# Performance work log

Hardware: AMD Instinct MI355X
Metric: run time of the kernel (lower is better)

The kernel has to match this reference:

```python
import jax, jax.numpy as jnp
import numpy as np

B, T, N, H = 256, 128, 512, 128  # batch, timesteps, input_size (driving series), hidden


def setup_inputs() -> dict:
    key = jax.random.key(0)
    ks = jax.random.split(key, 7)
    p = lambda k, shape: (jax.random.normal(k, shape, dtype=jnp.float32) * 0.05)
    return {
        "X": jax.random.normal(ks[0], (B, T, N), dtype=jnp.float32),
        # attention linear: in_features = 2H + T, out_features = 1 (stored as a vector + scalar bias)
        "attn_w": p(ks[1], (2 * H + T,)),
        "attn_b": p(ks[2], ()),
        # LSTM cell params, PyTorch layout/gate order (i, f, g, o)
        "w_ih": p(ks[3], (4 * H, N)),
        "w_hh": p(ks[4], (4 * H, H)),
        "b_ih": p(ks[5], (4 * H,)),
        "b_hh": p(ks[6], (4 * H,)),
    }


def reference(X, attn_w, attn_b, w_ih, w_hh, b_ih, b_hh):
    Bn, Tn, Nn = X.shape
    Hh = w_hh.shape[1]
    # split the single attention weight row into the h / s / X-row pieces of the concat
    w_h, w_s, w_x = attn_w[:Hh], attn_w[Hh:2 * Hh], attn_w[2 * Hh:]
    Xp = jnp.swapaxes(X, 1, 2)            # [B, N, T]  (X.permute(0,2,1))
    x_score = Xp @ w_x                    # [B, N], time-invariant part of attention logits

    def step(carry, x_t):                 # x_t: [B, N] = X[:, t, :]
        h, c = carry
        # logits[b,i] = w_h.h[b] + w_s.c[b] + w_x.Xp[b,i] + b  (== Linear on the concat)
        score = x_score + (h @ w_h + c @ w_s + attn_b)[:, None]   # [B, N]
        alpha = jax.nn.softmax(score, axis=1)
        x_tilde = alpha * x_t                                      # [B, N]
        gates = x_tilde @ w_ih.T + h @ w_hh.T + b_ih + b_hh        # [B, 4H]
        i, f, g, o = jnp.split(gates, 4, axis=1)
        c_new = jax.nn.sigmoid(f) * c + jax.nn.sigmoid(i) * jnp.tanh(g)
        h_new = jax.nn.sigmoid(o) * jnp.tanh(c_new)
        return (h_new, c_new), (x_tilde, h_new)

    h0 = jnp.zeros((Bn, Hh), X.dtype)
    (_, _), (Xt, Xe) = jax.lax.scan(step, (h0, h0), jnp.swapaxes(X, 0, 1))
    # scan stacks along time -> [T, B, .]; return [B, T, .]
    return jnp.swapaxes(Xt, 0, 1), jnp.swapaxes(Xe, 0, 1)
```

## Files before the change

kernel.cpp:

```cpp
#include <hip/hip_runtime.h>
#include <hip/hip_bf16.h>

#define Bb 256
#define Tt 128
#define Nn 512
#define Hh 128

typedef __attribute__((ext_vector_type(4))) float floatx4;
typedef __attribute__((ext_vector_type(8))) short short8;
typedef _Float16 h2v_t __attribute__((ext_vector_type(2)));

__device__ __forceinline__ unsigned short f2bf(float f) {
  unsigned u = __float_as_uint(f);
  u += 0x7fffu + ((u >> 16) & 1u);
  return (unsigned short)(u >> 16);
}

__device__ __forceinline__ float sigmoid_fast(float x) {
  return __builtin_amdgcn_rcpf(1.f + __expf(-x));
}
__device__ __forceinline__ float tanh_fast(float x) {
  float e = __expf(2.f * x);
  return 1.f - 2.f * __builtin_amdgcn_rcpf(e + 1.f);
}

__device__ __forceinline__ void lds_barrier() {
  asm volatile("s_waitcnt lgkmcnt(0)" ::: "memory");
  __builtin_amdgcn_s_barrier();
  asm volatile("" ::: "memory");
}

__device__ __forceinline__ void async_load16(const void* g, void* lds) {
  __builtin_amdgcn_global_load_lds(
      (const __attribute__((address_space(1))) unsigned int*)g,
      (__attribute__((address_space(3))) unsigned int*)lds, 16, 0, 0);
}

#if __has_builtin(__builtin_amdgcn_fdot2)
#define FDOT2(a, b, c) __builtin_amdgcn_fdot2((a), (b), (c), false)
#else
__device__ __forceinline__ float fdot2_sw(h2v_t a, h2v_t b, float c) {
  return fmaf((float)a.x, (float)b.x, fmaf((float)a.y, (float)b.y, (c)));
}
#define FDOT2(a, b, c) fdot2_sw((a), (b), (c))
#endif

template <int CTRL>
__device__ __forceinline__ float qperm(float x) {
#if __has_builtin(__builtin_amdgcn_update_dpp)
  return __uint_as_float((unsigned)__builtin_amdgcn_update_dpp(
      0, (int)__float_as_uint(x), CTRL, 0xf, 0xf, true));
#else
  return __shfl_xor(x, CTRL == 0xB1 ? 1 : 2, 64);
#endif
}

__global__ void prep_kernel(const float* __restrict__ w_ih,
                            const float* __restrict__ b_ih,
                            const float* __restrict__ b_hh,
                            unsigned short* __restrict__ wb,
                            float* __restrict__ bias) {
  int i = blockIdx.x * 256 + threadIdx.x;
  if (i < 4 * Hh * Nn) wb[i] = f2bf(w_ih[i]);
  if (i < 4 * Hh) bias[i] = b_ih[i] + b_hh[i];
}

__global__ __launch_bounds__(512) void alpha_kernel(const float* __restrict__ X,
                                                    const float* __restrict__ attn_w,
                                                    float* __restrict__ alpha) {
  int b = blockIdx.x;
  int tid = threadIdx.x;
  int c = tid & 127;
  int tp = tid >> 7;
  const float4* Xb = (const float4*)(X + (size_t)b * Tt * Nn) + c;
  const float* wx = attn_w + 2 * Hh;

  float4 acc = {0.f, 0.f, 0.f, 0.f};
#pragma unroll 8
  for (int tt = 0; tt < 32; ++tt) {
    int t = tp * 32 + tt;
    float4 x = Xb[(size_t)t * 128];
    float w = wx[t];
    acc.x = fmaf(x.x, w, acc.x);
    acc.y = fmaf(x.y, w, acc.y);
    acc.z = fmaf(x.z, w, acc.z);
    acc.w = fmaf(x.w, w, acc.w);
  }

  __shared__ float4 s4[512];
  __shared__ float sred[128];
  s4[tid] = acc;
  __syncthreads();

  float4 sc = {0.f, 0.f, 0.f, 0.f};
  if (tid < 128) {
    float4 a = s4[tid], b2 = s4[tid + 128], c2 = s4[tid + 256], d = s4[tid + 384];
    sc.x = a.x + b2.x + c2.x + d.x;
    sc.y = a.y + b2.y + c2.y + d.y;
    sc.z = a.z + b2.z + c2.z + d.z;
    sc.w = a.w + b2.w + c2.w + d.w;
    sred[tid] = fmaxf(fmaxf(sc.x, sc.y), fmaxf(sc.z, sc.w));
  }
  __syncthreads();
  for (int s = 64; s > 0; s >>= 1) {
    if (tid < s) sred[tid] = fmaxf(sred[tid], sred[tid + s]);
    __syncthreads();
  }
  float m = sred[0];
  __syncthreads();

  float4 e4 = {0.f, 0.f, 0.f, 0.f};
  if (tid < 128) {
    e4.x = __expf(sc.x - m);
    e4.y = __expf(sc.y - m);
    e4.z = __expf(sc.z - m);
    e4.w = __expf(sc.w - m);
    sred[tid] = e4.x + e4.y + e4.z + e4.w;
  }
  __syncthreads();
  for (int s = 64; s > 0; s >>= 1) {
    if (tid < s) sred[tid] += sred[tid + s];
    __syncthreads();
  }
  float inv = 1.f / sred[0];
  if (tid < 128) {
    float4 out;
    out.x = e4.x * inv; out.y = e4.y * inv; out.z = e4.z * inv; out.w = e4.w * inv;
    ((float4*)(alpha + (size_t)b * Nn))[tid] = out;
  }
}

__global__ __launch_bounds__(256) void scale_kernel(const float* __restrict__ X,
                                                    const float* __restrict__ alpha,
                                                    float* __restrict__ Xt,
                                                    unsigned short* __restrict__ xtb) {
  size_t i = (size_t)blockIdx.x * 256 + threadIdx.x;
  size_t e = i * 4;
  int n = (int)(e & (Nn - 1));
  int brow = (int)(e >> 9);
  int b = brow >> 7;
  float4 x = ((const float4*)X)[i];
  float4 a = *(const float4*)(alpha + (size_t)b * Nn + n);
  float4 y;
  y.x = x.x * a.x; y.y = x.y * a.y; y.z = x.z * a.z; y.w = x.w * a.w;
  ((float4*)Xt)[i] = y;
  ushort4 u;
  u.x = f2bf(y.x); u.y = f2bf(y.y); u.z = f2bf(y.z); u.w = f2bf(y.w);
  ((ushort4*)xtb)[i] = u;
}

#define GBK 64

__global__ __launch_bounds__(256) void gemm_bt(const unsigned short* __restrict__ A,
                                               const unsigned short* __restrict__ Bw,
                                               const float* __restrict__ bias,
                                               float* __restrict__ C) {
  __shared__ __align__(16) unsigned short As[128 * 64];
  __shared__ __align__(16) unsigned short Bs[128 * 64];
  const int K = 512, NO = 512;
  int tid = threadIdx.x;
  int lane = tid & 63;
  int wave = tid >> 6;
  int wm = wave & 1, wn = wave >> 1;
  int l15 = lane & 15;
  int quad = lane >> 4;
  int mtile = blockIdx.x, ntile = blockIdx.y;

  floatx4 acc[4][4];
#pragma unroll
  for (int i = 0; i < 4; ++i)
#pragma unroll
    for (int j = 0; j < 4; ++j) acc[i][j] = (floatx4){0.f, 0.f, 0.f, 0.f};

  int lr = lane >> 3;
  int lc = (lane & 7) ^ lr;
  const size_t lane_goff = (size_t)lr * K + lc * 8;
  const size_t abase = (size_t)mtile * 128 * K + lane_goff;
  const size_t bbase = (size_t)ntile * 128 * K + lane_goff;
  int sw = (quad ^ (l15 & 7)) * 8;

  for (int kb = 0; kb < K; kb += GBK) {
#pragma unroll
    for (int slot = 0; slot < 4; ++slot) {
      int r0 = slot * 32 + wave * 8;
      async_load16(A + abase + (size_t)r0 * K + kb, &As[r0 * 64]);
      async_load16(Bw + bbase + (size_t)r0 * K + kb, &Bs[r0 * 64]);
    }
    __syncthreads();
#pragma unroll
    for (int kh = 0; kh < 2; ++kh) {
      int sc = sw ^ (kh * 32);
      short8 af[4], bf[4];
#pragma unroll
      for (int i = 0; i < 4; ++i)
        af[i] = *(const short8*)(&As[(wm * 64 + i * 16 + l15) * 64 + sc]);
#pragma unroll
      for (int j = 0; j < 4; ++j)
        bf[j] = *(const short8*)(&Bs[(wn * 64 + j * 16 + l15) * 64 + sc]);
#pragma unroll
      for (int i = 0; i < 4; ++i)
#pragma unroll
        for (int j = 0; j < 4; ++j)
          acc[i][j] = __builtin_amdgcn_mfma_f32_16x16x32_bf16(af[i], bf[j], acc[i][j], 0, 0, 0);
    }
    __syncthreads();
  }

  int m0 = mtile * 128 + wm * 64;
  int n0 = ntile * 128 + wn * 64;
#pragma unroll
  for (int j = 0; j < 4; ++j) {
    int col = n0 + j * 16 + l15;
    float bsum = bias[col];
#pragma unroll
    for (int i = 0; i < 4; ++i) {
      int row = m0 + i * 16 + quad * 4;
#pragma unroll
      for (int r = 0; r < 4; ++r)
        C[(size_t)(row + r) * NO + col] = acc[i][j][r] + bsum;
    }
  }
}

__global__ __launch_bounds__(512, 1) void lstm_kernel(const float* __restrict__ G,
                                                      const float* __restrict__ w_hh,
                                                      float* __restrict__ Xe) {
  int b = blockIdx.x;
  int tid = threadIdx.x;
  int u = tid >> 2;
  int q = tid & 3;

  h2v_t wreg[4][16];
#pragma unroll
  for (int f = 0; f < 4; ++f) {
    const float4* wr = (const float4*)(w_hh + ((size_t)(f * 128 + u) * 128 + q * 32));
#pragma unroll
    for (int i = 0; i < 8; ++i) {
      float4 v = wr[i];
      wreg[f][2 * i]     = (h2v_t){(_Float16)v.x, (_Float16)v.y};
      wreg[f][2 * i + 1] = (h2v_t){(_Float16)v.z, (_Float16)v.w};
    }
  }

  __shared__ __align__(16) unsigned short h2[2][128];
  if (tid < 128) h2[0][tid] = 0;
  __syncthreads();

  const float* Gb = G + (size_t)b * Tt * 512 + q * 128 + u;
  float* Xeb = Xe + (size_t)b * Tt * Hh;

  float gcur = Gb[0];
  float gnext = Gb[512];
  float c0 = 0.f;

#define H2F(W) __builtin_bit_cast(h2v_t, (W))

  for (int t = 0; t < Tt; ++t) {
    int cur = t & 1;
    const uint4* hp = (const uint4*)(&h2[cur][0]) + q * 4;
    uint4 ha = hp[0], hb = hp[1], hc = hp[2], hd = hp[3];

    float g_this = gcur;
    gcur = gnext;
    if (t + 2 < Tt) gnext = Gb[(size_t)(t + 2) * 512];

    float pg0 = (q == 0) ? g_this : 0.f;
    float pg1 = (q == 1) ? g_this : 0.f;
    float pg2 = (q == 2) ? g_this : 0.f;
    float pg3 = (q == 3) ? g_this : 0.f;

#define DOTK(HB, K2)                                                \
  {                                                                 \
    h2v_t hh = __builtin_bit_cast(h2v_t, (HB));                     \
    pg0 = FDOT2(hh, wreg[0][K2], pg0);                              \
    pg1 = FDOT2(hh, wreg[1][K2], pg1);                              \
    pg2 = FDOT2(hh, wreg[2][K2], pg2);                              \
    pg3 = FDOT2(hh, wreg[3][K2], pg3);                              \
  }
    DOTK(ha.x, 0)  DOTK(ha.y, 1)  DOTK(ha.z, 2)  DOTK(ha.w, 3)
    DOTK(hb.x, 4)  DOTK(hb.y, 5)  DOTK(hb.z, 6)  DOTK(hb.w, 7)
    DOTK(hc.x, 8)  DOTK(hc.y, 9)  DOTK(hc.z, 10) DOTK(hc.w, 11)
    DOTK(hd.x, 12) DOTK(hd.y, 13) DOTK(hd.z, 14) DOTK(hd.w, 15)
#undef DOTK

    pg0 += qperm<0xB1>(pg0); pg1 += qperm<0xB1>(pg1);
    pg2 += qperm<0xB1>(pg2); pg3 += qperm<0xB1>(pg3);
    pg0 += qperm<0x4E>(pg0); pg1 += qperm<0x4E>(pg1);
    pg2 += qperm<0x4E>(pg2); pg3 += qperm<0x4E>(pg3);

    float si = sigmoid_fast(pg0);
    float sf = sigmoid_fast(pg1);
    float tg = tanh_fast(pg2);
    float so = sigmoid_fast(pg3);
    c0 = sf * c0 + si * tg;
    float hv = so * tanh_fast(c0);

    if (q == 0) {
      Xeb[(size_t)t * Hh + u] = hv;
      h2[cur ^ 1][u] = __builtin_bit_cast(unsigned short, (_Float16)hv);
    }
    lds_barrier();
  }
#undef H2F
}

extern "C" void kernel_launch(void* const* d_in, const int* in_sizes, int n_in,
                              void* d_out, int out_size, void* d_ws, size_t ws_size,
                              hipStream_t stream) {
  const float* X      = (const float*)d_in[0];
  const float* attn_w = (const float*)d_in[1];
  const float* w_ih   = (const float*)d_in[3];
  const float* w_hh   = (const float*)d_in[4];
  const float* b_ih   = (const float*)d_in[5];
  const float* b_hh   = (const float*)d_in[6];

  float* Xt = (float*)d_out;
  float* Xe = (float*)d_out + (size_t)Bb * Tt * Nn;

  char* ws = (char*)d_ws;
  float*          alpha = (float*)(ws);
  float*          bias  = (float*)(ws + 524288);
  unsigned short* wb    = (unsigned short*)(ws + 526336);
  unsigned short* xtb   = (unsigned short*)(ws + 1050624);
  float*          G     = (float*)(ws + 34605056);

  prep_kernel<<<dim3(1024), dim3(256), 0, stream>>>(w_ih, b_ih, b_hh, wb, bias);
  alpha_kernel<<<dim3(Bb), dim3(512), 0, stream>>>(X, attn_w, alpha);
  scale_kernel<<<dim3(16384), dim3(256), 0, stream>>>(X, alpha, Xt, xtb);
  gemm_bt<<<dim3(256, 4), dim3(256), 0, stream>>>(xtb, wb, bias, G);
  lstm_kernel<<<dim3(Bb), dim3(512), 0, stream>>>(G, w_hh, Xe);
}
```

Before: 272.0 us.

## Fuse input-projection GEMM into LSTM kernel with producer/consumer warp specialization

Replaces the separate bf16 GEMM that writes the gate pre-activations G to global memory, and the recurrent LSTM kernel, with one 1024-thread block per batch element. Eight waves compute 16-timestep chunks of x_tilde @ w_ih^T into a double-buffered LDS tile. The other eight waves run the recurrence on the previous chunk, so the GEMM overlaps the serial LSTM steps and the G round-trip through HBM goes away. In exchange, every block reloads the full w_ih matrix from global/L2 for each chunk. It also uses about 148KB of LDS, limiting occupancy to one block per CU, and adds a block-wide barrier on every step.

```diff
diff --git a/kernel.cpp b/kernel.cpp
--- a/kernel.cpp
+++ b/kernel.cpp
@@ -22,12 +22,6 @@
 __device__ __forceinline__ float tanh_fast(float x) {
   float e = __expf(2.f * x);
   return 1.f - 2.f * __builtin_amdgcn_rcpf(e + 1.f);
-}
-
-__device__ __forceinline__ void lds_barrier() {
-  asm volatile("s_waitcnt lgkmcnt(0)" ::: "memory");
-  __builtin_amdgcn_s_barrier();
-  asm volatile("" ::: "memory");
 }
 
 __device__ __forceinline__ void async_load16(const void* g, void* lds) {
@@ -149,125 +143,135 @@
   ((ushort4*)xtb)[i] = u;
 }
 
-#define GBK 64
-
-__global__ __launch_bounds__(256) void gemm_bt(const unsigned short* __restrict__ A,
-                                               const unsigned short* __restrict__ Bw,
-                                               const float* __restrict__ bias,
-                                               float* __restrict__ C) {
-  __shared__ __align__(16) unsigned short As[128 * 64];
-  __shared__ __align__(16) unsigned short Bs[128 * 64];
-  const int K = 512, NO = 512;
+__global__ __launch_bounds__(1024, 4) void fused_kernel(
+    const unsigned short* __restrict__ xtb,
+    const unsigned short* __restrict__ wb,
+    const float* __restrict__ bias,
+    const float* __restrict__ w_hh,
+    float* __restrict__ Xe) {
+  int b = blockIdx.x;
   int tid = threadIdx.x;
+  int wid = tid >> 6;
+  const bool isG = wid >= 8;
   int lane = tid & 63;
-  int wave = tid >> 6;
-  int wm = wave & 1, wn = wave >> 1;
   int l15 = lane & 15;
   int quad = lane >> 4;
-  int mtile = blockIdx.x, ntile = blockIdx.y;
-
-  floatx4 acc[4][4];
-#pragma unroll
-  for (int i = 0; i < 4; ++i)
-#pragma unroll
-    for (int j = 0; j < 4; ++j) acc[i][j] = (floatx4){0.f, 0.f, 0.f, 0.f};
-
-  int lr = lane >> 3;
-  int lc = (lane & 7) ^ lr;
-  const size_t lane_goff = (size_t)lr * K + lc * 8;
-  const size_t abase = (size_t)mtile * 128 * K + lane_goff;
-  const size_t bbase = (size_t)ntile * 128 * K + lane_goff;
-  int sw = (quad ^ (l15 & 7)) * 8;
-
-  for (int kb = 0; kb < K; kb += GBK) {
-#pragma unroll
-    for (int slot = 0; slot < 4; ++slot) {
-      int r0 = slot * 32 + wave * 8;
-      async_load16(A + abase + (size_t)r0 * K + kb, &As[r0 * 64]);
-      async_load16(Bw + bbase + (size_t)r0 * K + kb, &Bs[r0 * 64]);
-    }
-    __syncthreads();
-#pragma unroll
-    for (int kh = 0; kh < 2; ++kh) {
-      int sc = sw ^ (kh * 32);
-      short8 af[4], bf[4];
-#pragma unroll
-      for (int i = 0; i < 4; ++i)
-        af[i] = *(const short8*)(&As[(wm * 64 + i * 16 + l15) * 64 + sc]);
-#pragma unroll
-      for (int j = 0; j < 4; ++j)
-        bf[j] = *(const short8*)(&Bs[(wn * 64 + j * 16 + l15) * 64 + sc]);
-#pragma unroll
-      for (int i = 0; i < 4; ++i)
-#pragma unroll
-        for (int j = 0; j < 4; ++j)
-          acc[i][j] = __builtin_amdgcn_mfma_f32_16x16x32_bf16(af[i], bf[j], acc[i][j], 0, 0, 0);
-    }
-    __syncthreads();
-  }
-
-  int m0 = mtile * 128 + wm * 64;
-  int n0 = ntile * 128 + wn * 64;
-#pragma unroll
-  for (int j = 0; j < 4; ++j) {
-    int col = n0 + j * 16 + l15;
-    float bsum = bias[col];
-#pragma unroll
-    for (int i = 0; i < 4; ++i) {
-      int row = m0 + i * 16 + quad * 4;
-#pragma unroll
-      for (int r = 0; r < 4; ++r)
-        C[(size_t)(row + r) * NO + col] = acc[i][j][r] + bsum;
-    }
-  }
-}
-
-__global__ __launch_bounds__(512, 1) void lstm_kernel(const float* __restrict__ G,
-                                                      const float* __restrict__ w_hh,
-                                                      float* __restrict__ Xe) {
-  int b = blockIdx.x;
-  int tid = threadIdx.x;
+
+  extern __shared__ char smem[];
+  unsigned short* Bs = (unsigned short*)smem;
+  unsigned short* As = (unsigned short*)(smem + 65536);
+  float*          Gq = (float*)(smem + 81920);
+  unsigned short* h2s = (unsigned short*)(smem + 147456);
+
   int u = tid >> 2;
   int q = tid & 3;
-
   h2v_t wreg[4][16];
-#pragma unroll
-  for (int f = 0; f < 4; ++f) {
-    const float4* wr = (const float4*)(w_hh + ((size_t)(f * 128 + u) * 128 + q * 32));
-#pragma unroll
-    for (int i = 0; i < 8; ++i) {
-      float4 v = wr[i];
-      wreg[f][2 * i]     = (h2v_t){(_Float16)v.x, (_Float16)v.y};
-      wreg[f][2 * i + 1] = (h2v_t){(_Float16)v.z, (_Float16)v.w};
+  float c0 = 0.f;
+  float* Xeb = Xe + (size_t)b * Tt * Hh;
+  if (!isG) {
+#pragma unroll
+    for (int f = 0; f < 4; ++f) {
+      const float4* wr = (const float4*)(w_hh + ((size_t)(f * 128 + u) * 128 + q * 32));
+#pragma unroll
+      for (int i = 0; i < 8; ++i) {
+        float4 v = wr[i];
+        wreg[f][2 * i]     = (h2v_t){(_Float16)v.x, (_Float16)v.y};
+        wreg[f][2 * i + 1] = (h2v_t){(_Float16)v.z, (_Float16)v.w};
+      }
     }
-  }
-
-  __shared__ __align__(16) unsigned short h2[2][128];
-  if (tid < 128) h2[0][tid] = 0;
-  __syncthreads();
-
-  const float* Gb = G + (size_t)b * Tt * 512 + q * 128 + u;
-  float* Xeb = Xe + (size_t)b * Tt * Hh;
-
-  float gcur = Gb[0];
-  float gnext = Gb[512];
-  float c0 = 0.f;
-
-#define H2F(W) __builtin_bit_cast(h2v_t, (W))
-
-  for (int t = 0; t < Tt; ++t) {
-    int cur = t & 1;
-    const uint4* hp = (const uint4*)(&h2[cur][0]) + q * 4;
-    uint4 ha = hp[0], hb = hp[1], hc = hp[2], hd = hp[3];
-
-    float g_this = gcur;
-    gcur = gnext;
-    if (t + 2 < Tt) gnext = Gb[(size_t)(t + 2) * 512];
-
-    float pg0 = (q == 0) ? g_this : 0.f;
-    float pg1 = (q == 1) ? g_this : 0.f;
-    float pg2 = (q == 2) ? g_this : 0.f;
-    float pg3 = (q == 3) ? g_this : 0.f;
+    if (tid < 128) h2s[tid] = 0;
+  }
+
+  int w8 = wid - 8;
+  int glane = tid - 512;
+  int bbase[8];
+  int aoff0 = 0, aoff1 = 0;
+  float bias4[4];
+  int pos8_0 = (0 * 4 + quad) ^ (l15 & 7);
+  int pos8_1 = (1 * 4 + quad) ^ (l15 & 7);
+  if (isG) {
+#pragma unroll
+    for (int s = 0; s < 8; ++s) {
+      int lc = s * 512 + glane;
+      int row = lc >> 3, pos = lc & 7;
+      int ch = pos ^ (row & 7);
+      bbase[s] = row * 512 + ch * 8;
+    }
+    {
+      int lc = glane;
+      int row = lc >> 6, pos = lc & 63;
+      int ch = (pos & ~7) | ((pos & 7) ^ (row & 7));
+      aoff0 = row * 512 + ch * 8;
+      lc = 512 + glane;
+      row = lc >> 6; pos = lc & 63;
+      ch = (pos & ~7) | ((pos & 7) ^ (row & 7));
+      aoff1 = row * 512 + ch * 8;
+    }
+#pragma unroll
+    for (int nf = 0; nf < 4; ++nf) bias4[nf] = bias[w8 * 64 + nf * 16 + l15];
+  }
+  floatx4 acc[4];
+
+  __syncthreads();
+
+  for (int c = 0; c < 9; ++c) {
+    const bool gact = isG && (c < 8);
+    const bool lact = (!isG) && (c >= 1);
+    const float* gsrc = Gq + (size_t)((c + 1) & 1) * 8192;
+    float* gdst = Gq + (size_t)(c & 1) * 8192;
+    const unsigned short* Asrc = xtb + (((size_t)b * 128 + c * 16) * 512);
+
+#pragma unroll 2
+    for (int i = 0; i < 16; ++i) {
+      if (gact) {
+        if ((i & 1) == 0) {
+          int kb = i >> 1;
+          if (i == 0) {
+            async_load16(Asrc + aoff0, &As[(w8 * 64) * 8]);
+            async_load16(Asrc + aoff1, &As[(512 + w8 * 64) * 8]);
+          }
+#pragma unroll
+          for (int s = 0; s < 8; ++s)
+            async_load16(wb + bbase[s] + kb * 64, &Bs[(s * 512 + w8 * 64) * 8]);
+        } else {
+          int kb = i >> 1;
+          if (kb == 0) {
+#pragma unroll
+            for (int nf = 0; nf < 4; ++nf) acc[nf] = (floatx4){0.f, 0.f, 0.f, 0.f};
+          }
+          short8 af0 = *(const short8*)(&As[l15 * 512 + (kb * 8 + pos8_0) * 8]);
+          short8 af1 = *(const short8*)(&As[l15 * 512 + (kb * 8 + pos8_1) * 8]);
+#pragma unroll
+          for (int nf = 0; nf < 4; ++nf) {
+            int brow = (w8 * 64 + nf * 16 + l15) * 64;
+            short8 bf0 = *(const short8*)(&Bs[brow + pos8_0 * 8]);
+            short8 bf1 = *(const short8*)(&Bs[brow + pos8_1 * 8]);
+            acc[nf] = __builtin_amdgcn_mfma_f32_16x16x32_bf16(af0, bf0, acc[nf], 0, 0, 0);
+            acc[nf] = __builtin_amdgcn_mfma_f32_16x16x32_bf16(af1, bf1, acc[nf], 0, 0, 0);
+          }
+          if (i == 15) {
+#pragma unroll
+            for (int nf = 0; nf < 4; ++nf) {
+              int col = w8 * 64 + nf * 16 + l15;
+#pragma unroll
+              for (int r = 0; r < 4; ++r)
+                gdst[(quad * 4 + r) * 512 + col] = acc[nf][r] + bias4[nf];
+            }
+          }
+        }
+      }
+
+      if (lact) {
+        int t = (c - 1) * 16 + i;
+        int cur = i & 1;
+        const uint4* hp = (const uint4*)(&h2s[cur * 128]) + q * 4;
+        uint4 ha = hp[0], hb = hp[1], hc = hp[2], hd = hp[3];
+        float g_this = gsrc[i * 512 + q * 128 + u];
+
+        float pg0 = (q == 0) ? g_this : 0.f;
+        float pg1 = (q == 1) ? g_this : 0.f;
+        float pg2 = (q == 2) ? g_this : 0.f;
+        float pg3 = (q == 3) ? g_this : 0.f;
 
 #define DOTK(HB, K2)                                                \
   {                                                                 \
@@ -277,31 +281,39 @@
     pg2 = FDOT2(hh, wreg[2][K2], pg2);                              \
     pg3 = FDOT2(hh, wreg[3][K2], pg3);                              \
   }
-    DOTK(ha.x, 0)  DOTK(ha.y, 1)  DOTK(ha.z, 2)  DOTK(ha.w, 3)
-    DOTK(hb.x, 4)  DOTK(hb.y, 5)  DOTK(hb.z, 6)  DOTK(hb.w, 7)
-    DOTK(hc.x, 8)  DOTK(hc.y, 9)  DOTK(hc.z, 10) DOTK(hc.w, 11)
-    DOTK(hd.x, 12) DOTK(hd.y, 13) DOTK(hd.z, 14) DOTK(hd.w, 15)
+        DOTK(ha.x, 0)  DOTK(ha.y, 1)  DOTK(ha.z, 2)  DOTK(ha.w, 3)
+        DOTK(hb.x, 4)  DOTK(hb.y, 5)  DOTK(hb.z, 6)  DOTK(hb.w, 7)
+        DOTK(hc.x, 8)  DOTK(hc.y, 9)  DOTK(hc.z, 10) DOTK(hc.w, 11)
+        DOTK(hd.x, 12) DOTK(hd.y, 13) DOTK(hd.z, 14) DOTK(hd.w, 15)
 #undef DOTK
 
-    pg0 += qperm<0xB1>(pg0); pg1 += qperm<0xB1>(pg1);
-    pg2 += qperm<0xB1>(pg2); pg3 += qperm<0xB1>(pg3);
-    pg0 += qperm<0x4E>(pg0); pg1 += qperm<0x4E>(pg1);
-    pg2 += qperm<0x4E>(pg2); pg3 += qperm<0x4E>(pg3);
-
-    float si = sigmoid_fast(pg0);
-    float sf = sigmoid_fast(pg1);
-    float tg = tanh_fast(pg2);
-    float so = sigmoid_fast(pg3);
-    c0 = sf * c0 + si * tg;
-    float hv = so * tanh_fast(c0);
-
-    if (q == 0) {
-      Xeb[(size_t)t * Hh + u] = hv;
-      h2[cur ^ 1][u] = __builtin_bit_cast(unsigned short, (_Float16)hv);
+        pg0 += qperm<0xB1>(pg0); pg1 += qperm<0xB1>(pg1);
+        pg2 += qperm<0xB1>(pg2); pg3 += qperm<0xB1>(pg3);
+        pg0 += qperm<0x4E>(pg0); pg1 += qperm<0x4E>(pg1);
+        pg2 += qperm<0x4E>(pg2); pg3 += qperm<0x4E>(pg3);
+
+        float si = sigmoid_fast(pg0);
+        float sf = sigmoid_fast(pg1);
+        float tg = tanh_fast(pg2);
+        float so = sigmoid_fast(pg3);
+        c0 = sf * c0 + si * tg;
+        float hv = so * tanh_fast(c0);
+
+        if (q == 0) {
+          Xeb[(size_t)t * Hh + u] = hv;
+          h2s[(cur ^ 1) * 128 + u] = __builtin_bit_cast(unsigned short, (_Float16)hv);
+        }
+      }
+
+      if (isG) {
+        asm volatile("s_waitcnt vmcnt(0) lgkmcnt(0)" ::: "memory");
+      } else {
+        asm volatile("s_waitcnt lgkmcnt(0)" ::: "memory");
+      }
+      __builtin_amdgcn_s_barrier();
+      asm volatile("" ::: "memory");
     }
-    lds_barrier();
-  }
-#undef H2F
+  }
 }
 
 extern "C" void kernel_launch(void* const* d_in, const int* in_sizes, int n_in,
@@ -322,11 +334,12 @@
   float*          bias  = (float*)(ws + 524288);
   unsigned short* wb    = (unsigned short*)(ws + 526336);
   unsigned short* xtb   = (unsigned short*)(ws + 1050624);
-  float*          G     = (float*)(ws + 34605056);
+
+  hipFuncSetAttribute(reinterpret_cast<const void*>(fused_kernel),
+                      hipFuncAttributeMaxDynamicSharedMemorySize, 147968);
 
   prep_kernel<<<dim3(1024), dim3(256), 0, stream>>>(w_ih, b_ih, b_hh, wb, bias);
   alpha_kernel<<<dim3(Bb), dim3(512), 0, stream>>>(X, attn_w, alpha);
   scale_kernel<<<dim3(16384), dim3(256), 0, stream>>>(X, alpha, Xt, xtb);
-  gemm_bt<<<dim3(256, 4), dim3(256), 0, stream>>>(xtb, wb, bias, G);
-  lstm_kernel<<<dim3(Bb), dim3(512), 0, stream>>>(G, w_hh, Xe);
-}
+  fused_kernel<<<dim3(Bb), dim3(1024), 147968, stream>>>(xtb, wb, bias, w_hh, Xe);
+}
```

Measured after the change: 370.9 us. +36.4%, slower.
